# Kernel optimization log

Measured on AMD Instinct MI355X. Metric: run time of the kernel, lower is better.

Reference implementation:

```python
import jax, jax.numpy as jnp
import numpy as np

N_NODES = 100000
N_EDGES = 800000
N_ETYPES = 5
IN_DIM = 23
HID_DIM = 128
OUT_DIM = 64
NUM_GRAPHS = 64


def setup_inputs() -> dict:
    key = jax.random.key(0)
    ks = jax.random.split(key, 8)
    feat = jax.random.normal(ks[0], (N_NODES, IN_DIM), dtype=jnp.float32)
    src = jax.random.randint(ks[1], (N_ETYPES, N_EDGES), 0, N_NODES, dtype=jnp.int32)
    dst = jax.random.randint(ks[2], (N_ETYPES, N_EDGES), 0, N_NODES, dtype=jnp.int32)
    graph_ids = jnp.sort(jax.random.randint(ks[3], (N_NODES,), 0, NUM_GRAPHS, dtype=jnp.int32))
    W1 = jax.random.normal(ks[4], (N_ETYPES, IN_DIM, HID_DIM), dtype=jnp.float32) * 0.1
    b1 = jnp.zeros((N_ETYPES, HID_DIM), dtype=jnp.float32)
    W2 = jax.random.normal(ks[5], (N_ETYPES, HID_DIM, OUT_DIM), dtype=jnp.float32) * 0.1
    b2 = jnp.zeros((N_ETYPES, OUT_DIM), dtype=jnp.float32)
    return {"feat": feat, "src": src, "dst": dst, "graph_ids": graph_ids,
            "W1": W1, "b1": b1, "W2": W2, "b2": b2}


def _hetero_sage_layer(h, src, dst, W, b):
    """HeteroGraphConv of SAGEConv(aggregator='gcn') summed over edge types.
    gcn aggregator: h_neigh[i] = (sum_{j->i} h[j] + h[i]) / (in_deg(i) + 1);
    per-etype output = h_neigh @ W_e + b_e; combine with sum."""
    n = h.shape[0]
    out = jnp.zeros((n, W.shape[-1]), dtype=h.dtype)
    ones_e = jnp.ones((src.shape[1],), dtype=h.dtype)
    for e in range(N_ETYPES):
        deg = jax.ops.segment_sum(ones_e, dst[e], num_segments=n)          # [N]
        agg = jax.ops.segment_sum(h[src[e]], dst[e], num_segments=n)       # [N, D]
        h_neigh = (agg + h) / (deg + 1.0)[:, None]
        out = out + h_neigh @ W[e] + b[e]
    return out


def reference(feat, src, dst, graph_ids, W1, b1, W2, b2):
    # layer 1: in_dim -> hid, relu (dropout in eval mode = identity)
    h = jax.nn.relu(_hetero_sage_layer(feat, src, dst, W1, b1))
    # layer 2: hid -> out (no activation)
    h = _hetero_sage_layer(h, src, dst, W2, b2)
    # dgl.mean_nodes: per-graph mean over nodes
    counts = jax.ops.segment_sum(jnp.ones((h.shape[0],), h.dtype), graph_ids,
                                 num_segments=NUM_GRAPHS)
    sums = jax.ops.segment_sum(h, graph_ids, num_segments=NUM_GRAPHS)
    return sums / jnp.maximum(counts, 1.0)[:, None]
```

## Files before the change

kernel.cpp:

```cpp
#include <hip/hip_runtime.h>

#define N_NODES   100000
#define N_EDGES   800000
#define N_ETYPES  5
#define IN_DIM    23
#define FPAD      32
#define HID_DIM   128
#define OUT_DIM   64
#define NUM_GRAPHS 64
#define NBKT      391
#define PBLK      125
#define CHUNK     6400
#define PN        (N_ETYPES*NBKT*PBLK)
#define SCAN_NBLK ((PN + 1023) / 1024)
#define TOT_EDGES (N_ETYPES*N_EDGES)
#define BKT_CAP   3072
#define ASTR      136
#define A1STR     40


__device__ __forceinline__ unsigned short f2bf(float x) {
    unsigned u = __float_as_uint(x);
    unsigned r = (u + 0x7FFFu + ((u >> 16) & 1u)) >> 16;
    return (unsigned short)r;
}
__device__ __forceinline__ float bf2f(unsigned short h) {
    return __uint_as_float(((unsigned)h) << 16);
}

typedef __attribute__((ext_vector_type(8))) short bf16x8;
typedef __attribute__((ext_vector_type(4))) float f32x4;
typedef __attribute__((ext_vector_type(2))) float f32x2;

__global__ __launch_bounds__(256) void cvt_feat_k(const float* __restrict__ feat,
                                                  unsigned short* __restrict__ fb32) {
    int i = blockIdx.x * 256 + threadIdx.x;
    if (i < N_NODES * FPAD) {
        int n = i >> 5, d = i & 31;
        fb32[i] = (d < IN_DIM) ? f2bf(feat[n * IN_DIM + d]) : (unsigned short)0;
    }
}

__global__ __launch_bounds__(256) void cvt_w_k(const float* __restrict__ W1,
                                               const float* __restrict__ b1,
                                               const float* __restrict__ W2,
                                               unsigned short* __restrict__ w1tb,
                                               unsigned short* __restrict__ w2tb,
                                               float* __restrict__ b1s) {
    int i = blockIdx.x * 256 + threadIdx.x;
    if (i < N_ETYPES * OUT_DIM * HID_DIM) {
        int e = i / (OUT_DIM * HID_DIM);
        int r = i - e * (OUT_DIM * HID_DIM);
        int n = r >> 7, k = r & 127;
        w2tb[i] = f2bf(W2[(e * HID_DIM + k) * OUT_DIM + n]);
    }
    if (i < N_ETYPES * HID_DIM * 32) {
        int e = i / (HID_DIM * 32);
        int r = i - e * (HID_DIM * 32);
        int n = r >> 5, k = r & 31;
        w1tb[i] = (k < IN_DIM) ? f2bf(W1[e * IN_DIM * HID_DIM + k * HID_DIM + n])
                               : (unsigned short)0;
    }
    if (i < HID_DIM) {
        float s = 0.f;
        for (int e = 0; e < N_ETYPES; e++) s += b1[e * HID_DIM + i];
        b1s[i] = s;
    }
}

__global__ __launch_bounds__(256) void part1_k(const int* __restrict__ dst,
                                               int* __restrict__ hp) {
    __shared__ int hist[NBKT];
    int e = blockIdx.y, blk = blockIdx.x, t = threadIdx.x;
    for (int b = t; b < NBKT; b += 256) hist[b] = 0;
    __syncthreads();
    const int* dp = dst + e * N_EDGES + blk * CHUNK;
    for (int k = t; k < CHUNK; k += 256) atomicAdd(&hist[dp[k] >> 8], 1);
    __syncthreads();
    for (int b = t; b < NBKT; b += 256) hp[(e * NBKT + b) * PBLK + blk] = hist[b];
}

__global__ __launch_bounds__(256) void scan1_k(const int* __restrict__ in,
                                               int* __restrict__ out,
                                               int* __restrict__ bsum) {
    __shared__ int ls[256];
    int t = threadIdx.x;
    int base = blockIdx.x * 1024 + t * 4;
    int v[4]; int s = 0;
    for (int j = 0; j < 4; j++) { int i = base + j; v[j] = (i < PN) ? in[i] : 0; s += v[j]; }
    ls[t] = s; __syncthreads();
    for (int o = 1; o < 256; o <<= 1) {
        int x = (t >= o) ? ls[t - o] : 0;
        __syncthreads();
        ls[t] += x;
        __syncthreads();
    }
    int run = (t > 0) ? ls[t - 1] : 0;
    if (t == 255) bsum[blockIdx.x] = ls[255];
    for (int j = 0; j < 4; j++) { int i = base + j; if (i < PN) out[i] = run; run += v[j]; }
}

__global__ __launch_bounds__(256) void scan2_k(int* __restrict__ bsum) {
    __shared__ int ls[256];
    int t = threadIdx.x;
    int v = (t < SCAN_NBLK) ? bsum[t] : 0;
    ls[t] = v; __syncthreads();
    for (int o = 1; o < 256; o <<= 1) {
        int x = (t >= o) ? ls[t - o] : 0;
        __syncthreads();
        ls[t] += x;
        __syncthreads();
    }
    if (t < SCAN_NBLK) bsum[t] = (t > 0) ? ls[t - 1] : 0;
}

__global__ __launch_bounds__(256) void scan3_k(int* __restrict__ off,
                                               const int* __restrict__ bsum) {
    int i = blockIdx.x * 256 + threadIdx.x;
    if (i < PN) off[i] += bsum[i >> 10];
}

__global__ __launch_bounds__(256) void part2_k(const int* __restrict__ src,
                                               const int* __restrict__ dst,
                                               const int* __restrict__ off,
                                               unsigned* __restrict__ ep) {
    __shared__ int cur[NBKT];
    int e = blockIdx.y, blk = blockIdx.x, t = threadIdx.x;
    for (int b = t; b < NBKT; b += 256) cur[b] = off[(e * NBKT + b) * PBLK + blk];
    __syncthreads();
    const int* dp = dst + e * N_EDGES + blk * CHUNK;
    const int* sp = src + e * N_EDGES + blk * CHUNK;
    for (int k = t; k < CHUNK; k += 256) {
        int d = dp[k], s = sp[k];
        int b = d >> 8;
        int pos = atomicAdd(&cur[b], 1);
        ep[pos] = (unsigned)s | ((unsigned)(d & 255) << 24);
    }
}

__global__ __launch_bounds__(256) void sort_k(const int* __restrict__ off,
                                              const unsigned* __restrict__ ep,
                                              unsigned* __restrict__ csr,
                                              int* __restrict__ noff,
                                              int* __restrict__ degn,
                                              float* __restrict__ inv) {
    __shared__ unsigned recs[BKT_CAP];
    __shared__ int hist[256];
    __shared__ int scn[256];
    __shared__ int curp[256];
    int b = blockIdx.x, e = blockIdx.y, t = threadIdx.x;
    int lin = (e * NBKT + b) * PBLK;
    int S = off[lin];
    int E = (lin == PN - PBLK) ? TOT_EDGES : off[lin + PBLK];
    int cnt = E - S;
    hist[t] = 0;
    __syncthreads();
    for (int i = t; i < cnt; i += 256) {
        unsigned r = ep[S + i];
        recs[i] = r;
        atomicAdd(&hist[r >> 24], 1);
    }
    __syncthreads();
    scn[t] = hist[t];
    __syncthreads();
    for (int o = 1; o < 256; o <<= 1) {
        int x = (t >= o) ? scn[t - o] : 0;
        __syncthreads();
        scn[t] += x;
        __syncthreads();
    }
    int excl = scn[t] - hist[t];
    curp[t] = excl;
    int n = b * 256 + t;
    if (n < N_NODES) {
        noff[e * N_NODES + n] = S + excl;
        degn[e * N_NODES + n] = hist[t];
        inv[e * N_NODES + n]  = 1.f / (float)(hist[t] + 1);
    }
    __syncthreads();
    for (int i = t; i < cnt; i += 256) {
        unsigned r = recs[i];
        int pos = atomicAdd(&curp[r >> 24], 1);
        csr[S + pos] = r & 0xFFFFFFu;
    }
}

__global__ __launch_bounds__(256) void agg1_k(const int* __restrict__ noff,
                                              const int* __restrict__ degn,
                                              const unsigned* __restrict__ csr,
                                              const unsigned short* __restrict__ fb32,
                                              const float* __restrict__ inv,
                                              unsigned short* __restrict__ agg1b) {
    int e = blockIdx.y;
    int t = threadIdx.x;
    int lane = t & 15;
    int n = blockIdx.x * 16 + (t >> 4);
    int idx = e * N_NODES + n;
    int st = noff[idx];
    int cnt = degn[idx];
    ushort2 sv = *(const ushort2*)&fb32[n * FPAD + lane * 2];
    float a0 = bf2f(sv.x), a1 = bf2f(sv.y);
    int k = 0;
    for (; k + 3 < cnt; k += 4) {
        int s0 = csr[st + k];
        int s1 = csr[st + k + 1];
        int s2 = csr[st + k + 2];
        int s3 = csr[st + k + 3];
        ushort2 v0 = *(const ushort2*)&fb32[s0 * FPAD + lane * 2];
        ushort2 v1 = *(const ushort2*)&fb32[s1 * FPAD + lane * 2];
        ushort2 v2 = *(const ushort2*)&fb32[s2 * FPAD + lane * 2];
        ushort2 v3 = *(const ushort2*)&fb32[s3 * FPAD + lane * 2];
        a0 += bf2f(v0.x) + bf2f(v1.x) + bf2f(v2.x) + bf2f(v3.x);
        a1 += bf2f(v0.y) + bf2f(v1.y) + bf2f(v2.y) + bf2f(v3.y);
    }
    for (; k < cnt; k++) {
        int s0 = csr[st + k];
        ushort2 v0 = *(const ushort2*)&fb32[s0 * FPAD + lane * 2];
        a0 += bf2f(v0.x);
        a1 += bf2f(v0.y);
    }
    float iv = inv[idx];
    ushort2 o; o.x = f2bf(a0 * iv); o.y = f2bf(a1 * iv);
    *(ushort2*)&agg1b[(size_t)idx * 32 + lane * 2] = o;
}

__global__ __launch_bounds__(256) void gemm12_k(const unsigned short* __restrict__ agg1b,
                                                const unsigned short* __restrict__ w1tb,
                                                const float* __restrict__ b1s,
                                                const unsigned short* __restrict__ w2tb,
                                                unsigned char* __restrict__ t2f8) {
    __shared__ unsigned short H1s[64 * ASTR];
    __shared__ unsigned short Wt2[64 * ASTR];
    unsigned short* As1 = Wt2;
    unsigned short* Wt1 = Wt2 + 64 * A1STR;
    int t = threadIdx.x;
    int node0 = blockIdx.x * 64;
    int w = t >> 6, lane = t & 63;
    int m = lane & 15, quad = lane >> 4;

    f32x4 acc[8];
    for (int nt = 0; nt < 8; nt++) {
        float bb = b1s[nt * 16 + m];
        f32x4 c = {bb, bb, bb, bb};
        acc[nt] = c;
    }
    for (int e = 0; e < N_ETYPES; e++) {
        __syncthreads();
        for (int j = t; j < 64 * 8; j += 256) {
            int n = j >> 3, c4 = (j & 7) * 4;
            int gn = node0 + n;
            int cn = gn < N_NODES ? gn : N_NODES - 1;
            *(ushort4*)&As1[n * A1STR + c4] =
                *(const ushort4*)&agg1b[(size_t)(e * N_NODES + cn) * 32 + c4];
        }
        for (int j = t; j < 128 * 8; j += 256) {
            int n = j >> 3, c4 = (j & 7) * 4;
            *(ushort4*)&Wt1[n * A1STR + c4] =
                *(const ushort4*)&w1tb[(size_t)(e * HID_DIM + n) * 32 + c4];
        }
        __syncthreads();
        bf16x8 a = *(const bf16x8*)&As1[(w * 16 + m) * A1STR + quad * 8];
        for (int nt = 0; nt < 8; nt++) {
            bf16x8 b = *(const bf16x8*)&Wt1[(nt * 16 + m) * A1STR + quad * 8];
            acc[nt] = __builtin_amdgcn_mfma_f32_16x16x32_bf16(a, b, acc[nt], 0, 0, 0);
        }
    }
    __syncthreads();
    for (int nt = 0; nt < 8; nt++)
        for (int r = 0; r < 4; r++)
            H1s[(w * 16 + quad * 4 + r) * ASTR + nt * 16 + m] =
                f2bf(fmaxf(acc[nt][r], 0.f));
    __syncthreads();

    bf16x8 a2[4];
    for (int ks = 0; ks < 4; ks++)
        a2[ks] = *(const bf16x8*)&H1s[(w * 16 + m) * ASTR + ks * 32 + quad * 8];
    for (int e = 0; e < N_ETYPES; e++) {
        __syncthreads();
        for (int j = t; j < 64 * 32; j += 256) {
            int n = j >> 5, c4 = (j & 31) * 4;
            *(ushort4*)&Wt2[n * ASTR + c4] =
                *(const ushort4*)&w2tb[(e * OUT_DIM + n) * HID_DIM + c4];
        }
        __syncthreads();
        unsigned char* out = t2f8 + (size_t)e * N_NODES * OUT_DIM;
        for (int nt = 0; nt < 4; nt++) {
            f32x4 c = {0.f, 0.f, 0.f, 0.f};
            for (int ks = 0; ks < 4; ks++) {
                bf16x8 b = *(const bf16x8*)&Wt2[(nt * 16 + m) * ASTR + ks * 32 + quad * 8];
                c = __builtin_amdgcn_mfma_f32_16x16x32_bf16(a2[ks], b, c, 0, 0, 0);
            }
            for (int r = 0; r < 4; r++) {
                int gn = node0 + w * 16 + quad * 4 + r;
                if (gn < N_NODES) {
                    int p = __builtin_amdgcn_cvt_pk_fp8_f32(c[r], c[r], 0, false);
                    out[(size_t)gn * OUT_DIM + nt * 16 + m] = (unsigned char)(p & 0xFF);
                }
            }
        }
    }
}

__global__ __launch_bounds__(256) void gather2_k(const int* __restrict__ noff,
                                                 const int* __restrict__ degn,
                                                 const float* __restrict__ inv,
                                                 const unsigned* __restrict__ csr,
                                                 const unsigned char* __restrict__ t2f8,
                                                 const int* __restrict__ gid,
                                                 float* __restrict__ gsum) {
    __shared__ float red[32 * 64];
    __shared__ int slotl[32];
    int b = blockIdx.x, qb = blockIdx.y, t = threadIdx.x;
    int lane = t & 7, ng = t >> 3;
    int nbase = b * 256 + qb * 32;
    int gbase = nbase < N_NODES ? nbase : N_NODES - 1;
    int g0 = gid[gbase];
    if (t < 32) {
        int nn = nbase + t;
        slotl[t] = (nn < N_NODES) ? gid[nn] - g0 : -1;
    }
    __syncthreads();
    int n = nbase + ng;
    float f0=0,f1=0,f2=0,f3=0,f4=0,f5=0,f6=0,f7=0;
    if (n < N_NODES) {
        for (int e = 0; e < N_ETYPES; e++) {
            const unsigned char* base = t2f8 + (size_t)e * N_NODES * OUT_DIM;
            int idx = e * N_NODES + n;
            int st = noff[idx];
            int cnt = degn[idx];
            float iv = inv[idx];
            uint2 rv = *(const uint2*)&base[(size_t)n * OUT_DIM + lane * 8];
            f32x2 l0 = __builtin_amdgcn_cvt_pk_f32_fp8((int)rv.x, false);
            f32x2 h0 = __builtin_amdgcn_cvt_pk_f32_fp8((int)rv.x, true);
            f32x2 l1 = __builtin_amdgcn_cvt_pk_f32_fp8((int)rv.y, false);
            f32x2 h1 = __builtin_amdgcn_cvt_pk_f32_fp8((int)rv.y, true);
            float a0=l0.x,a1=l0.y,a2=h0.x,a3=h0.y,a4=l1.x,a5=l1.y,a6=h1.x,a7=h1.y;
            int k = 0;
            for (; k + 3 < cnt; k += 4) {
                int sA = csr[st + k];
                int sB = csr[st + k + 1];
                int sC = csr[st + k + 2];
                int sD = csr[st + k + 3];
                uint2 rA = *(const uint2*)&base[(size_t)sA * OUT_DIM + lane * 8];
                uint2 rB = *(const uint2*)&base[(size_t)sB * OUT_DIM + lane * 8];
                uint2 rC = *(const uint2*)&base[(size_t)sC * OUT_DIM + lane * 8];
                uint2 rD = *(const uint2*)&base[(size_t)sD * OUT_DIM + lane * 8];
                f32x2 v;
                v = __builtin_amdgcn_cvt_pk_f32_fp8((int)rA.x, false); a0+=v.x; a1+=v.y;
                v = __builtin_amdgcn_cvt_pk_f32_fp8((int)rA.x, true);  a2+=v.x; a3+=v.y;
                v = __builtin_amdgcn_cvt_pk_f32_fp8((int)rA.y, false); a4+=v.x; a5+=v.y;
                v = __builtin_amdgcn_cvt_pk_f32_fp8((int)rA.y, true);  a6+=v.x; a7+=v.y;
                v = __builtin_amdgcn_cvt_pk_f32_fp8((int)rB.x, false); a0+=v.x; a1+=v.y;
                v = __builtin_amdgcn_cvt_pk_f32_fp8((int)rB.x, true);  a2+=v.x; a3+=v.y;
                v = __builtin_amdgcn_cvt_pk_f32_fp8((int)rB.y, false); a4+=v.x; a5+=v.y;
                v = __builtin_amdgcn_cvt_pk_f32_fp8((int)rB.y, true);  a6+=v.x; a7+=v.y;
                v = __builtin_amdgcn_cvt_pk_f32_fp8((int)rC.x, false); a0+=v.x; a1+=v.y;
                v = __builtin_amdgcn_cvt_pk_f32_fp8((int)rC.x, true);  a2+=v.x; a3+=v.y;
                v = __builtin_amdgcn_cvt_pk_f32_fp8((int)rC.y, false); a4+=v.x; a5+=v.y;
                v = __builtin_amdgcn_cvt_pk_f32_fp8((int)rC.y, true);  a6+=v.x; a7+=v.y;
                v = __builtin_amdgcn_cvt_pk_f32_fp8((int)rD.x, false); a0+=v.x; a1+=v.y;
                v = __builtin_amdgcn_cvt_pk_f32_fp8((int)rD.x, true);  a2+=v.x; a3+=v.y;
                v = __builtin_amdgcn_cvt_pk_f32_fp8((int)rD.y, false); a4+=v.x; a5+=v.y;
                v = __builtin_amdgcn_cvt_pk_f32_fp8((int)rD.y, true);  a6+=v.x; a7+=v.y;
            }
            for (; k < cnt; k++) {
                int sA = csr[st + k];
                uint2 rA = *(const uint2*)&base[(size_t)sA * OUT_DIM + lane * 8];
                f32x2 v;
                v = __builtin_amdgcn_cvt_pk_f32_fp8((int)rA.x, false); a0+=v.x; a1+=v.y;
                v = __builtin_amdgcn_cvt_pk_f32_fp8((int)rA.x, true);  a2+=v.x; a3+=v.y;
                v = __builtin_amdgcn_cvt_pk_f32_fp8((int)rA.y, false); a4+=v.x; a5+=v.y;
                v = __builtin_amdgcn_cvt_pk_f32_fp8((int)rA.y, true);  a6+=v.x; a7+=v.y;
            }
            f0+=iv*a0; f1+=iv*a1; f2+=iv*a2; f3+=iv*a3;
            f4+=iv*a4; f5+=iv*a5; f6+=iv*a6; f7+=iv*a7;
        }
    }
    int slot = slotl[ng];
    if (slot > 3 && n < N_NODES) {
        int gbase8 = (g0 + slot) * 64 + lane * 8;
        atomicAdd(&gsum[gbase8 + 0], f0); atomicAdd(&gsum[gbase8 + 1], f1);
        atomicAdd(&gsum[gbase8 + 2], f2); atomicAdd(&gsum[gbase8 + 3], f3);
        atomicAdd(&gsum[gbase8 + 4], f4); atomicAdd(&gsum[gbase8 + 5], f5);
        atomicAdd(&gsum[gbase8 + 6], f6); atomicAdd(&gsum[gbase8 + 7], f7);
        f0=f1=f2=f3=f4=f5=f6=f7=0.f;
    }
    *(float4*)&red[ng * 64 + lane * 8]     = make_float4(f0, f1, f2, f3);
    *(float4*)&red[ng * 64 + lane * 8 + 4] = make_float4(f4, f5, f6, f7);
    __syncthreads();
    int slot2 = t >> 6, d = t & 63;
    float s = 0.f;
    for (int j = 0; j < 32; j++)
        s += (slotl[j] == slot2) ? red[j * 64 + d] : 0.f;
    int g = g0 + slot2;
    if (g < NUM_GRAPHS) atomicAdd(&gsum[g * 64 + d], s);
}

__global__ __launch_bounds__(256) void gcnt_k(const int* __restrict__ gid,
                                              float* __restrict__ gcnt) {
    __shared__ int h[NUM_GRAPHS];
    int b = blockIdx.x, t = threadIdx.x;
    if (t < NUM_GRAPHS) h[t] = 0;
    __syncthreads();
    int n = b * 256 + t;
    if (n < N_NODES) atomicAdd(&h[gid[n]], 1);
    __syncthreads();
    if (t < NUM_GRAPHS && h[t] > 0) atomicAdd(&gcnt[t], (float)h[t]);
}

__global__ __launch_bounds__(256) void final_k(const float* __restrict__ gsum,
                                               const float* __restrict__ gcnt,
                                               const float* __restrict__ b2,
                                               float* __restrict__ out) {
    int idx = blockIdx.x * 256 + threadIdx.x;
    if (idx >= NUM_GRAPHS * OUT_DIM) return;
    int d = idx & 63;
    float B2 = 0.f;
    for (int e = 0; e < N_ETYPES; e++) B2 += b2[e * OUT_DIM + d];
    float c = gcnt[idx >> 6];
    out[idx] = (gsum[idx] + c * B2) / fmaxf(c, 1.0f);
}

extern "C" void kernel_launch(void* const* d_in, const int* in_sizes, int n_in,
                              void* d_out, int out_size, void* d_ws, size_t ws_size,
                              hipStream_t stream) {
    const float* feat = (const float*)d_in[0];
    const int*   src  = (const int*)d_in[1];
    const int*   dst  = (const int*)d_in[2];
    const int*   gid  = (const int*)d_in[3];
    const float* W1   = (const float*)d_in[4];
    const float* b1   = (const float*)d_in[5];
    const float* W2   = (const float*)d_in[6];
    const float* b2   = (const float*)d_in[7];

    float* ws = (float*)d_ws;
    int*            HP   = (int*)ws;
    int*            OFFP = (int*)ws + 245000;
    int*            BSUM = (int*)ws + 490000;
    float*          INV  = ws + 490512;
    int*            NOFF = (int*)ws + 990512;
    int*            DEGN = (int*)ws + 1490512;
    unsigned short* FB32 = (unsigned short*)(ws + 1990512);
    float*          GSUM = ws + 3590512;
    float*          GCNT = ws + 3594608;
    unsigned*       EP   = (unsigned*)(ws + 3595000);
    unsigned short* AGG1B= (unsigned short*)(ws + 7595000);
    unsigned char*  T2F8 = (unsigned char*)(ws + 3595000);
    T2F8 = (unsigned char*)(ws + 15595000);
    unsigned*       CSR  = (unsigned*)(ws + 23595000);
    unsigned short* W2TB = (unsigned short*)(ws + 27595000);
    unsigned short* W1TB = (unsigned short*)(ws + 27615480);
    float*          B1S  = ws + 27625720;

    hipMemsetAsync(GSUM, 0, (size_t)(4096 + 64) * sizeof(float), stream);

    cvt_feat_k<<<(N_NODES * FPAD + 255) / 256, 256, 0, stream>>>(feat, FB32);
    cvt_w_k<<<(N_ETYPES * OUT_DIM * HID_DIM + 255) / 256, 256, 0, stream>>>(
        W1, b1, W2, W1TB, W2TB, B1S);
    part1_k<<<dim3(PBLK, N_ETYPES), 256, 0, stream>>>(dst, HP);
    scan1_k<<<SCAN_NBLK, 256, 0, stream>>>(HP, OFFP, BSUM);
    scan2_k<<<1, 256, 0, stream>>>(BSUM);
    scan3_k<<<(PN + 255) / 256, 256, 0, stream>>>(OFFP, BSUM);
    part2_k<<<dim3(PBLK, N_ETYPES), 256, 0, stream>>>(src, dst, OFFP, EP);
    sort_k<<<dim3(NBKT, N_ETYPES), 256, 0, stream>>>(OFFP, EP, CSR, NOFF, DEGN, INV);

    agg1_k<<<dim3(6250, N_ETYPES), 256, 0, stream>>>(NOFF, DEGN, CSR, FB32, INV, AGG1B);
    gemm12_k<<<(N_NODES + 63) / 64, 256, 0, stream>>>(AGG1B, W1TB, B1S, W2TB, T2F8);
    gather2_k<<<dim3(NBKT, 8), 256, 0, stream>>>(NOFF, DEGN, INV, CSR, T2F8, gid, GSUM);

    gcnt_k<<<391, 256, 0, stream>>>(gid, GCNT);
    final_k<<<16, 256, 0, stream>>>(GSUM, GCNT, b2, (float*)d_out);
}
```

Before: 416.7 us.

## Reorder layer-2 aggregation and mean-pool before the W2 GEMM via source-bucketed pooling

Layer 2 and the per-graph mean are linear, so the change pools h1 directly into a per-etype, per-graph matrix M. Each source node's contribution is weighted by inv-degree of its destination, with self loops added as virtual edges. The 64x128 pooled matrix is then multiplied by W2 in a small final kernel. This removes the per-node layer-2 GEMM, the fp8 T2 intermediate and the gather over 64-wide rows. In exchange it adds a second partitioning pass keyed by source, writes a bf16 h1 buffer, runs an in-shared-memory sort by graph id, and does scattered 128-wide reads of h1 with many float atomics into M.

```diff
diff --git a/kernel.cpp b/kernel.cpp
--- a/kernel.cpp
+++ b/kernel.cpp
@@ -11,11 +11,14 @@
 #define NBKT      391
 #define PBLK      125
 #define CHUNK     6400
+#define VEDGES    900000
+#define CHUNK2    7200
 #define PN        (N_ETYPES*NBKT*PBLK)
-#define SCAN_NBLK ((PN + 1023) / 1024)
+#define PN2TOT    (2*PN)
+#define SCAN_NBLK ((PN2TOT + 1023) / 1024)
 #define TOT_EDGES (N_ETYPES*N_EDGES)
+#define TOT2      (TOT_EDGES + N_ETYPES*VEDGES)
 #define BKT_CAP   3072
-#define ASTR      136
 #define A1STR     40
 
 
@@ -30,7 +33,6 @@
 
 typedef __attribute__((ext_vector_type(8))) short bf16x8;
 typedef __attribute__((ext_vector_type(4))) float f32x4;
-typedef __attribute__((ext_vector_type(2))) float f32x2;
 
 __global__ __launch_bounds__(256) void cvt_feat_k(const float* __restrict__ feat,
                                                   unsigned short* __restrict__ fb32) {
@@ -43,17 +45,9 @@
 
 __global__ __launch_bounds__(256) void cvt_w_k(const float* __restrict__ W1,
                                                const float* __restrict__ b1,
-                                               const float* __restrict__ W2,
                                                unsigned short* __restrict__ w1tb,
-                                               unsigned short* __restrict__ w2tb,
                                                float* __restrict__ b1s) {
     int i = blockIdx.x * 256 + threadIdx.x;
-    if (i < N_ETYPES * OUT_DIM * HID_DIM) {
-        int e = i / (OUT_DIM * HID_DIM);
-        int r = i - e * (OUT_DIM * HID_DIM);
-        int n = r >> 7, k = r & 127;
-        w2tb[i] = f2bf(W2[(e * HID_DIM + k) * OUT_DIM + n]);
-    }
     if (i < N_ETYPES * HID_DIM * 32) {
         int e = i / (HID_DIM * 32);
         int r = i - e * (HID_DIM * 32);
@@ -68,16 +62,27 @@
     }
 }
 
-__global__ __launch_bounds__(256) void part1_k(const int* __restrict__ dst,
+__global__ __launch_bounds__(256) void part1_k(const int* __restrict__ src,
+                                               const int* __restrict__ dst,
                                                int* __restrict__ hp) {
-    __shared__ int hist[NBKT];
+    __shared__ int hd[NBKT];
+    __shared__ int hs[NBKT];
     int e = blockIdx.y, blk = blockIdx.x, t = threadIdx.x;
-    for (int b = t; b < NBKT; b += 256) hist[b] = 0;
+    for (int b = t; b < NBKT; b += 256) { hd[b] = 0; hs[b] = 0; }
     __syncthreads();
     const int* dp = dst + e * N_EDGES + blk * CHUNK;
-    for (int k = t; k < CHUNK; k += 256) atomicAdd(&hist[dp[k] >> 8], 1);
-    __syncthreads();
-    for (int b = t; b < NBKT; b += 256) hp[(e * NBKT + b) * PBLK + blk] = hist[b];
+    for (int k = t; k < CHUNK; k += 256) atomicAdd(&hd[dp[k] >> 8], 1);
+    const int* sp = src + e * N_EDGES;
+    for (int k = t; k < CHUNK2; k += 256) {
+        int i = blk * CHUNK2 + k;
+        int s = (i < N_EDGES) ? sp[i] : (i - N_EDGES);
+        atomicAdd(&hs[s >> 8], 1);
+    }
+    __syncthreads();
+    for (int b = t; b < NBKT; b += 256) {
+        hp[(e * NBKT + b) * PBLK + blk] = hd[b];
+        hp[PN + (e * NBKT + b) * PBLK + blk] = hs[b];
+    }
 }
 
 __global__ __launch_bounds__(256) void scan1_k(const int* __restrict__ in,
@@ -87,7 +92,7 @@
     int t = threadIdx.x;
     int base = blockIdx.x * 1024 + t * 4;
     int v[4]; int s = 0;
-    for (int j = 0; j < 4; j++) { int i = base + j; v[j] = (i < PN) ? in[i] : 0; s += v[j]; }
+    for (int j = 0; j < 4; j++) { int i = base + j; v[j] = (i < PN2TOT) ? in[i] : 0; s += v[j]; }
     ls[t] = s; __syncthreads();
     for (int o = 1; o < 256; o <<= 1) {
         int x = (t >= o) ? ls[t - o] : 0;
@@ -97,15 +102,15 @@
     }
     int run = (t > 0) ? ls[t - 1] : 0;
     if (t == 255) bsum[blockIdx.x] = ls[255];
-    for (int j = 0; j < 4; j++) { int i = base + j; if (i < PN) out[i] = run; run += v[j]; }
-}
-
-__global__ __launch_bounds__(256) void scan2_k(int* __restrict__ bsum) {
-    __shared__ int ls[256];
+    for (int j = 0; j < 4; j++) { int i = base + j; if (i < PN2TOT) out[i] = run; run += v[j]; }
+}
+
+__global__ __launch_bounds__(512) void scan2_k(int* __restrict__ bsum) {
+    __shared__ int ls[512];
     int t = threadIdx.x;
     int v = (t < SCAN_NBLK) ? bsum[t] : 0;
     ls[t] = v; __syncthreads();
-    for (int o = 1; o < 256; o <<= 1) {
+    for (int o = 1; o < 512; o <<= 1) {
         int x = (t >= o) ? ls[t - o] : 0;
         __syncthreads();
         ls[t] += x;
@@ -117,7 +122,7 @@
 __global__ __launch_bounds__(256) void scan3_k(int* __restrict__ off,
                                                const int* __restrict__ bsum) {
     int i = blockIdx.x * 256 + threadIdx.x;
-    if (i < PN) off[i] += bsum[i >> 10];
+    if (i < PN2TOT) off[i] += bsum[i >> 10];
 }
 
 __global__ __launch_bounds__(256) void part2_k(const int* __restrict__ src,
@@ -151,7 +156,7 @@
     int b = blockIdx.x, e = blockIdx.y, t = threadIdx.x;
     int lin = (e * NBKT + b) * PBLK;
     int S = off[lin];
-    int E = (lin == PN - PBLK) ? TOT_EDGES : off[lin + PBLK];
+    int E = off[lin + PBLK];
     int cnt = E - S;
     hist[t] = 0;
     __syncthreads();
@@ -182,6 +187,31 @@
         unsigned r = recs[i];
         int pos = atomicAdd(&curp[r >> 24], 1);
         csr[S + pos] = r & 0xFFFFFFu;
+    }
+}
+
+__global__ __launch_bounds__(256) void part2b_k(const int* __restrict__ src,
+                                                const int* __restrict__ dst,
+                                                const int* __restrict__ gid,
+                                                const float* __restrict__ inv,
+                                                const int* __restrict__ off,
+                                                unsigned* __restrict__ ep) {
+    __shared__ int cur[NBKT];
+    int e = blockIdx.y, blk = blockIdx.x, t = threadIdx.x;
+    for (int b = t; b < NBKT; b += 256) cur[b] = off[PN + (e * NBKT + b) * PBLK + blk];
+    __syncthreads();
+    const int* sp = src + e * N_EDGES;
+    const int* dp = dst + e * N_EDGES;
+    for (int k = t; k < CHUNK2; k += 256) {
+        int i = blk * CHUNK2 + k;
+        int s, d;
+        if (i < N_EDGES) { s = sp[i]; d = dp[i]; }
+        else             { s = i - N_EDGES; d = s; }
+        unsigned g = (unsigned)gid[d];
+        unsigned wv = f2bf(inv[e * N_NODES + d]);
+        int b = s >> 8;
+        int pos = atomicAdd(&cur[b], 1);
+        ep[pos] = ((unsigned)(s & 255) << 24) | (g << 16) | wv;
     }
 }
 
@@ -224,15 +254,12 @@
     *(ushort2*)&agg1b[(size_t)idx * 32 + lane * 2] = o;
 }
 
-__global__ __launch_bounds__(256) void gemm12_k(const unsigned short* __restrict__ agg1b,
-                                                const unsigned short* __restrict__ w1tb,
-                                                const float* __restrict__ b1s,
-                                                const unsigned short* __restrict__ w2tb,
-                                                unsigned char* __restrict__ t2f8) {
-    __shared__ unsigned short H1s[64 * ASTR];
-    __shared__ unsigned short Wt2[64 * ASTR];
-    unsigned short* As1 = Wt2;
-    unsigned short* Wt1 = Wt2 + 64 * A1STR;
+__global__ __launch_bounds__(256) void gemm1_k(const unsigned short* __restrict__ agg1b,
+                                               const unsigned short* __restrict__ w1tb,
+                                               const float* __restrict__ b1s,
+                                               unsigned short* __restrict__ h1b) {
+    __shared__ unsigned short As[64 * A1STR];
+    __shared__ unsigned short Wt[128 * A1STR];
     int t = threadIdx.x;
     int node0 = blockIdx.x * 64;
     int w = t >> 6, lane = t & 63;
@@ -250,150 +277,112 @@
             int n = j >> 3, c4 = (j & 7) * 4;
             int gn = node0 + n;
             int cn = gn < N_NODES ? gn : N_NODES - 1;
-            *(ushort4*)&As1[n * A1STR + c4] =
+            *(ushort4*)&As[n * A1STR + c4] =
                 *(const ushort4*)&agg1b[(size_t)(e * N_NODES + cn) * 32 + c4];
         }
         for (int j = t; j < 128 * 8; j += 256) {
             int n = j >> 3, c4 = (j & 7) * 4;
-            *(ushort4*)&Wt1[n * A1STR + c4] =
+            *(ushort4*)&Wt[n * A1STR + c4] =
                 *(const ushort4*)&w1tb[(size_t)(e * HID_DIM + n) * 32 + c4];
         }
         __syncthreads();
-        bf16x8 a = *(const bf16x8*)&As1[(w * 16 + m) * A1STR + quad * 8];
+        bf16x8 a = *(const bf16x8*)&As[(w * 16 + m) * A1STR + quad * 8];
         for (int nt = 0; nt < 8; nt++) {
-            bf16x8 b = *(const bf16x8*)&Wt1[(nt * 16 + m) * A1STR + quad * 8];
+            bf16x8 b = *(const bf16x8*)&Wt[(nt * 16 + m) * A1STR + quad * 8];
             acc[nt] = __builtin_amdgcn_mfma_f32_16x16x32_bf16(a, b, acc[nt], 0, 0, 0);
         }
     }
-    __syncthreads();
-    for (int nt = 0; nt < 8; nt++)
-        for (int r = 0; r < 4; r++)
-            H1s[(w * 16 + quad * 4 + r) * ASTR + nt * 16 + m] =
-                f2bf(fmaxf(acc[nt][r], 0.f));
-    __syncthreads();
-
-    bf16x8 a2[4];
-    for (int ks = 0; ks < 4; ks++)
-        a2[ks] = *(const bf16x8*)&H1s[(w * 16 + m) * ASTR + ks * 32 + quad * 8];
-    for (int e = 0; e < N_ETYPES; e++) {
-        __syncthreads();
-        for (int j = t; j < 64 * 32; j += 256) {
-            int n = j >> 5, c4 = (j & 31) * 4;
-            *(ushort4*)&Wt2[n * ASTR + c4] =
-                *(const ushort4*)&w2tb[(e * OUT_DIM + n) * HID_DIM + c4];
-        }
-        __syncthreads();
-        unsigned char* out = t2f8 + (size_t)e * N_NODES * OUT_DIM;
-        for (int nt = 0; nt < 4; nt++) {
-            f32x4 c = {0.f, 0.f, 0.f, 0.f};
-            for (int ks = 0; ks < 4; ks++) {
-                bf16x8 b = *(const bf16x8*)&Wt2[(nt * 16 + m) * ASTR + ks * 32 + quad * 8];
-                c = __builtin_amdgcn_mfma_f32_16x16x32_bf16(a2[ks], b, c, 0, 0, 0);
+    for (int nt = 0; nt < 8; nt++) {
+        for (int r = 0; r < 4; r++) {
+            int gn = node0 + w * 16 + quad * 4 + r;
+            if (gn < N_NODES)
+                h1b[(size_t)gn * HID_DIM + nt * 16 + m] = f2bf(fmaxf(acc[nt][r], 0.f));
+        }
+    }
+}
+
+__global__ __launch_bounds__(256) void spool_k(const int* __restrict__ offp,
+                                               const unsigned* __restrict__ ep,
+                                               const unsigned short* __restrict__ h1b,
+                                               float* __restrict__ M) {
+    __shared__ unsigned recs[BKT_CAP];
+    __shared__ unsigned srt[BKT_CAP];
+    __shared__ int hist[64];
+    __shared__ int boff[65];
+    __shared__ int curs[64];
+    int q = blockIdx.x, e = blockIdx.y, t = threadIdx.x;
+    int w = t >> 6, lane = t & 63;
+    float a0[16], a1[16];
+    #pragma unroll
+    for (int gi = 0; gi < 16; gi++) { a0[gi] = 0.f; a1[gi] = 0.f; }
+
+    for (int bi = 0; bi < 4; bi++) {
+        int b = q * 4 + bi;
+        if (b >= NBKT) break;
+        int lin = PN + (e * NBKT + b) * PBLK;
+        int S = offp[lin];
+        int E = (lin + PBLK == PN2TOT) ? TOT2 : offp[lin + PBLK];
+        int cnt = E - S;
+        if (cnt > BKT_CAP) cnt = BKT_CAP;
+        if (t < 64) hist[t] = 0;
+        __syncthreads();
+        for (int i = t; i < cnt; i += 256) {
+            unsigned r = ep[S + i];
+            recs[i] = r;
+            atomicAdd(&hist[(r >> 16) & 63], 1);
+        }
+        __syncthreads();
+        if (t == 0) {
+            int run = 0;
+            for (int g = 0; g < 64; g++) { boff[g] = run; run += hist[g]; }
+            boff[64] = run;
+        }
+        __syncthreads();
+        if (t < 64) curs[t] = boff[t];
+        __syncthreads();
+        for (int i = t; i < cnt; i += 256) {
+            unsigned r = recs[i];
+            int pos = atomicAdd(&curs[(r >> 16) & 63], 1);
+            srt[pos] = r;
+        }
+        __syncthreads();
+        int nodebase = b * 256;
+        #pragma unroll
+        for (int gi = 0; gi < 16; gi++) {
+            int g = w * 16 + gi;
+            int lo = boff[g], hi = boff[g + 1];
+            int i = lo;
+            for (; i + 3 < hi; i += 4) {
+                unsigned r0 = srt[i], r1 = srt[i + 1], r2 = srt[i + 2], r3 = srt[i + 3];
+                float w0 = bf2f((unsigned short)(r0 & 0xFFFF));
+                float w1 = bf2f((unsigned short)(r1 & 0xFFFF));
+                float w2 = bf2f((unsigned short)(r2 & 0xFFFF));
+                float w3 = bf2f((unsigned short)(r3 & 0xFFFF));
+                ushort2 v0 = *(const ushort2*)&h1b[(size_t)(nodebase + (r0 >> 24)) * HID_DIM + lane * 2];
+                ushort2 v1 = *(const ushort2*)&h1b[(size_t)(nodebase + (r1 >> 24)) * HID_DIM + lane * 2];
+                ushort2 v2 = *(const ushort2*)&h1b[(size_t)(nodebase + (r2 >> 24)) * HID_DIM + lane * 2];
+                ushort2 v3 = *(const ushort2*)&h1b[(size_t)(nodebase + (r3 >> 24)) * HID_DIM + lane * 2];
+                a0[gi] += w0 * bf2f(v0.x) + w1 * bf2f(v1.x)
+                        + w2 * bf2f(v2.x) + w3 * bf2f(v3.x);
+                a1[gi] += w0 * bf2f(v0.y) + w1 * bf2f(v1.y)
+                        + w2 * bf2f(v2.y) + w3 * bf2f(v3.y);
             }
-            for (int r = 0; r < 4; r++) {
-                int gn = node0 + w * 16 + quad * 4 + r;
-                if (gn < N_NODES) {
-                    int p = __builtin_amdgcn_cvt_pk_fp8_f32(c[r], c[r], 0, false);
-                    out[(size_t)gn * OUT_DIM + nt * 16 + m] = (unsigned char)(p & 0xFF);
-                }
+            for (; i < hi; i++) {
+                unsigned r0 = srt[i];
+                float w0 = bf2f((unsigned short)(r0 & 0xFFFF));
+                ushort2 v0 = *(const ushort2*)&h1b[(size_t)(nodebase + (r0 >> 24)) * HID_DIM + lane * 2];
+                a0[gi] += w0 * bf2f(v0.x);
+                a1[gi] += w0 * bf2f(v0.y);
             }
         }
-    }
-}
-
-__global__ __launch_bounds__(256) void gather2_k(const int* __restrict__ noff,
-                                                 const int* __restrict__ degn,
-                                                 const float* __restrict__ inv,
-                                                 const unsigned* __restrict__ csr,
-                                                 const unsigned char* __restrict__ t2f8,
-                                                 const int* __restrict__ gid,
-                                                 float* __restrict__ gsum) {
-    __shared__ float red[32 * 64];
-    __shared__ int slotl[32];
-    int b = blockIdx.x, qb = blockIdx.y, t = threadIdx.x;
-    int lane = t & 7, ng = t >> 3;
-    int nbase = b * 256 + qb * 32;
-    int gbase = nbase < N_NODES ? nbase : N_NODES - 1;
-    int g0 = gid[gbase];
-    if (t < 32) {
-        int nn = nbase + t;
-        slotl[t] = (nn < N_NODES) ? gid[nn] - g0 : -1;
-    }
-    __syncthreads();
-    int n = nbase + ng;
-    float f0=0,f1=0,f2=0,f3=0,f4=0,f5=0,f6=0,f7=0;
-    if (n < N_NODES) {
-        for (int e = 0; e < N_ETYPES; e++) {
-            const unsigned char* base = t2f8 + (size_t)e * N_NODES * OUT_DIM;
-            int idx = e * N_NODES + n;
-            int st = noff[idx];
-            int cnt = degn[idx];
-            float iv = inv[idx];
-            uint2 rv = *(const uint2*)&base[(size_t)n * OUT_DIM + lane * 8];
-            f32x2 l0 = __builtin_amdgcn_cvt_pk_f32_fp8((int)rv.x, false);
-            f32x2 h0 = __builtin_amdgcn_cvt_pk_f32_fp8((int)rv.x, true);
-            f32x2 l1 = __builtin_amdgcn_cvt_pk_f32_fp8((int)rv.y, false);
-            f32x2 h1 = __builtin_amdgcn_cvt_pk_f32_fp8((int)rv.y, true);
-            float a0=l0.x,a1=l0.y,a2=h0.x,a3=h0.y,a4=l1.x,a5=l1.y,a6=h1.x,a7=h1.y;
-            int k = 0;
-            for (; k + 3 < cnt; k += 4) {
-                int sA = csr[st + k];
-                int sB = csr[st + k + 1];
-                int sC = csr[st + k + 2];
-                int sD = csr[st + k + 3];
-                uint2 rA = *(const uint2*)&base[(size_t)sA * OUT_DIM + lane * 8];
-                uint2 rB = *(const uint2*)&base[(size_t)sB * OUT_DIM + lane * 8];
-                uint2 rC = *(const uint2*)&base[(size_t)sC * OUT_DIM + lane * 8];
-                uint2 rD = *(const uint2*)&base[(size_t)sD * OUT_DIM + lane * 8];
-                f32x2 v;
-                v = __builtin_amdgcn_cvt_pk_f32_fp8((int)rA.x, false); a0+=v.x; a1+=v.y;
-                v = __builtin_amdgcn_cvt_pk_f32_fp8((int)rA.x, true);  a2+=v.x; a3+=v.y;
-                v = __builtin_amdgcn_cvt_pk_f32_fp8((int)rA.y, false); a4+=v.x; a5+=v.y;
-                v = __builtin_amdgcn_cvt_pk_f32_fp8((int)rA.y, true);  a6+=v.x; a7+=v.y;
-                v = __builtin_amdgcn_cvt_pk_f32_fp8((int)rB.x, false); a0+=v.x; a1+=v.y;
-                v = __builtin_amdgcn_cvt_pk_f32_fp8((int)rB.x, true);  a2+=v.x; a3+=v.y;
-                v = __builtin_amdgcn_cvt_pk_f32_fp8((int)rB.y, false); a4+=v.x; a5+=v.y;
-                v = __builtin_amdgcn_cvt_pk_f32_fp8((int)rB.y, true);  a6+=v.x; a7+=v.y;
-                v = __builtin_amdgcn_cvt_pk_f32_fp8((int)rC.x, false); a0+=v.x; a1+=v.y;
-                v = __builtin_amdgcn_cvt_pk_f32_fp8((int)rC.x, true);  a2+=v.x; a3+=v.y;
-                v = __builtin_amdgcn_cvt_pk_f32_fp8((int)rC.y, false); a4+=v.x; a5+=v.y;
-                v = __builtin_amdgcn_cvt_pk_f32_fp8((int)rC.y, true);  a6+=v.x; a7+=v.y;
-                v = __builtin_amdgcn_cvt_pk_f32_fp8((int)rD.x, false); a0+=v.x; a1+=v.y;
-                v = __builtin_amdgcn_cvt_pk_f32_fp8((int)rD.x, true);  a2+=v.x; a3+=v.y;
-                v = __builtin_amdgcn_cvt_pk_f32_fp8((int)rD.y, false); a4+=v.x; a5+=v.y;
-                v = __builtin_amdgcn_cvt_pk_f32_fp8((int)rD.y, true);  a6+=v.x; a7+=v.y;
-            }
-            for (; k < cnt; k++) {
-                int sA = csr[st + k];
-                uint2 rA = *(const uint2*)&base[(size_t)sA * OUT_DIM + lane * 8];
-                f32x2 v;
-                v = __builtin_amdgcn_cvt_pk_f32_fp8((int)rA.x, false); a0+=v.x; a1+=v.y;
-                v = __builtin_amdgcn_cvt_pk_f32_fp8((int)rA.x, true);  a2+=v.x; a3+=v.y;
-                v = __builtin_amdgcn_cvt_pk_f32_fp8((int)rA.y, false); a4+=v.x; a5+=v.y;
-                v = __builtin_amdgcn_cvt_pk_f32_fp8((int)rA.y, true);  a6+=v.x; a7+=v.y;
-            }
-            f0+=iv*a0; f1+=iv*a1; f2+=iv*a2; f3+=iv*a3;
-            f4+=iv*a4; f5+=iv*a5; f6+=iv*a6; f7+=iv*a7;
-        }
-    }
-    int slot = slotl[ng];
-    if (slot > 3 && n < N_NODES) {
-        int gbase8 = (g0 + slot) * 64 + lane * 8;
-        atomicAdd(&gsum[gbase8 + 0], f0); atomicAdd(&gsum[gbase8 + 1], f1);
-        atomicAdd(&gsum[gbase8 + 2], f2); atomicAdd(&gsum[gbase8 + 3], f3);
-        atomicAdd(&gsum[gbase8 + 4], f4); atomicAdd(&gsum[gbase8 + 5], f5);
-        atomicAdd(&gsum[gbase8 + 6], f6); atomicAdd(&gsum[gbase8 + 7], f7);
-        f0=f1=f2=f3=f4=f5=f6=f7=0.f;
-    }
-    *(float4*)&red[ng * 64 + lane * 8]     = make_float4(f0, f1, f2, f3);
-    *(float4*)&red[ng * 64 + lane * 8 + 4] = make_float4(f4, f5, f6, f7);
-    __syncthreads();
-    int slot2 = t >> 6, d = t & 63;
-    float s = 0.f;
-    for (int j = 0; j < 32; j++)
-        s += (slotl[j] == slot2) ? red[j * 64 + d] : 0.f;
-    int g = g0 + slot2;
-    if (g < NUM_GRAPHS) atomicAdd(&gsum[g * 64 + d], s);
+        __syncthreads();
+    }
+    #pragma unroll
+    for (int gi = 0; gi < 16; gi++) {
+        int g = w * 16 + gi;
+        atomicAdd(&M[((size_t)e * 64 + g) * HID_DIM + lane * 2 + 0], a0[gi]);
+        atomicAdd(&M[((size_t)e * 64 + g) * HID_DIM + lane * 2 + 1], a1[gi]);
+    }
 }
 
 __global__ __launch_bounds__(256) void gcnt_k(const int* __restrict__ gid,
@@ -408,17 +397,23 @@
     if (t < NUM_GRAPHS && h[t] > 0) atomicAdd(&gcnt[t], (float)h[t]);
 }
 
-__global__ __launch_bounds__(256) void final_k(const float* __restrict__ gsum,
+__global__ __launch_bounds__(64) void final2_k(const float* __restrict__ M,
+                                               const float* __restrict__ W2,
+                                               const float* __restrict__ b2,
                                                const float* __restrict__ gcnt,
-                                               const float* __restrict__ b2,
                                                float* __restrict__ out) {
-    int idx = blockIdx.x * 256 + threadIdx.x;
-    if (idx >= NUM_GRAPHS * OUT_DIM) return;
-    int d = idx & 63;
+    int g = blockIdx.x, d = threadIdx.x;
+    float s = 0.f;
+    for (int e = 0; e < N_ETYPES; e++) {
+        const float* mrow = M + ((size_t)e * 64 + g) * HID_DIM;
+        const float* wmat = W2 + (size_t)e * HID_DIM * OUT_DIM;
+        for (int k = 0; k < HID_DIM; k++)
+            s += mrow[k] * wmat[k * OUT_DIM + d];
+    }
     float B2 = 0.f;
     for (int e = 0; e < N_ETYPES; e++) B2 += b2[e * OUT_DIM + d];
-    float c = gcnt[idx >> 6];
-    out[idx] = (gsum[idx] + c * B2) / fmaxf(c, 1.0f);
+    float c = gcnt[g];
+    out[g * OUT_DIM + d] = (s + c * B2) / fmaxf(c, 1.0f);
 }
 
 extern "C" void kernel_launch(void* const* d_in, const int* in_sizes, int n_in,
@@ -435,39 +430,37 @@
 
     float* ws = (float*)d_ws;
     int*            HP   = (int*)ws;
-    int*            OFFP = (int*)ws + 245000;
-    int*            BSUM = (int*)ws + 490000;
-    float*          INV  = ws + 490512;
-    int*            NOFF = (int*)ws + 990512;
-    int*            DEGN = (int*)ws + 1490512;
-    unsigned short* FB32 = (unsigned short*)(ws + 1990512);
-    float*          GSUM = ws + 3590512;
-    float*          GCNT = ws + 3594608;
-    unsigned*       EP   = (unsigned*)(ws + 3595000);
-    unsigned short* AGG1B= (unsigned short*)(ws + 7595000);
-    unsigned char*  T2F8 = (unsigned char*)(ws + 3595000);
-    T2F8 = (unsigned char*)(ws + 15595000);
-    unsigned*       CSR  = (unsigned*)(ws + 23595000);
-    unsigned short* W2TB = (unsigned short*)(ws + 27595000);
-    unsigned short* W1TB = (unsigned short*)(ws + 27615480);
-    float*          B1S  = ws + 27625720;
-
-    hipMemsetAsync(GSUM, 0, (size_t)(4096 + 64) * sizeof(float), stream);
+    int*            OFFP = (int*)ws + 490000;
+    int*            BSUM = (int*)ws + 980000;
+    float*          INV  = ws + 980512;
+    int*            NOFF = (int*)ws + 1480512;
+    int*            DEGN = (int*)ws + 1980512;
+    unsigned short* FB32 = (unsigned short*)(ws + 2480512);
+    float*          Mbuf = ws + 4080512;
+    float*          GCNT = ws + 4121472;
+    unsigned*       EP   = (unsigned*)(ws + 4121600);
+    unsigned*       CSR  = (unsigned*)(ws + 12621600);
+    unsigned short* AGG1B= (unsigned short*)(ws + 16621600);
+    unsigned short* H1B  = (unsigned short*)(ws + 24621600);
+    unsigned short* W1TB = (unsigned short*)(ws + 31021600);
+    float*          B1S  = ws + 31031840;
+
+    hipMemsetAsync(Mbuf, 0, (size_t)(40960 + 64 + 64) * sizeof(float), stream);
 
     cvt_feat_k<<<(N_NODES * FPAD + 255) / 256, 256, 0, stream>>>(feat, FB32);
-    cvt_w_k<<<(N_ETYPES * OUT_DIM * HID_DIM + 255) / 256, 256, 0, stream>>>(
-        W1, b1, W2, W1TB, W2TB, B1S);
-    part1_k<<<dim3(PBLK, N_ETYPES), 256, 0, stream>>>(dst, HP);
+    cvt_w_k<<<(N_ETYPES * HID_DIM * 32 + 255) / 256, 256, 0, stream>>>(W1, b1, W1TB, B1S);
+    part1_k<<<dim3(PBLK, N_ETYPES), 256, 0, stream>>>(src, dst, HP);
     scan1_k<<<SCAN_NBLK, 256, 0, stream>>>(HP, OFFP, BSUM);
-    scan2_k<<<1, 256, 0, stream>>>(BSUM);
-    scan3_k<<<(PN + 255) / 256, 256, 0, stream>>>(OFFP, BSUM);
+    scan2_k<<<1, 512, 0, stream>>>(BSUM);
+    scan3_k<<<(PN2TOT + 255) / 256, 256, 0, stream>>>(OFFP, BSUM);
     part2_k<<<dim3(PBLK, N_ETYPES), 256, 0, stream>>>(src, dst, OFFP, EP);
     sort_k<<<dim3(NBKT, N_ETYPES), 256, 0, stream>>>(OFFP, EP, CSR, NOFF, DEGN, INV);
+    part2b_k<<<dim3(PBLK, N_ETYPES), 256, 0, stream>>>(src, dst, gid, INV, OFFP, EP);
 
     agg1_k<<<dim3(6250, N_ETYPES), 256, 0, stream>>>(NOFF, DEGN, CSR, FB32, INV, AGG1B);
-    gemm12_k<<<(N_NODES + 63) / 64, 256, 0, stream>>>(AGG1B, W1TB, B1S, W2TB, T2F8);
-    gather2_k<<<dim3(NBKT, 8), 256, 0, stream>>>(NOFF, DEGN, INV, CSR, T2F8, gid, GSUM);
+    gemm1_k<<<(N_NODES + 63) / 64, 256, 0, stream>>>(AGG1B, W1TB, B1S, H1B);
+    spool_k<<<dim3(98, N_ETYPES), 256, 0, stream>>>(OFFP, EP, H1B, Mbuf);
 
     gcnt_k<<<391, 256, 0, stream>>>(gid, GCNT);
-    final_k<<<16, 256, 0, stream>>>(GSUM, GCNT, b2, (float*)d_out);
-}
+    final2_k<<<NUM_GRAPHS, 64, 0, stream>>>(Mbuf, W2, b2, GCNT, (float*)d_out);
+}
```

Result: slower. 695.9 us (+67.0%).
